# Optimization experiments

Measured on AMD Instinct MI355X. Metric: run time of the kernel, lower is better.

Reference implementation:

```python
import jax, jax.numpy as jnp
import numpy as np

D_MODEL, D_K, D_V, N_HEADS = 1024, 64, 64, 16


def setup_inputs() -> dict:
    key = jax.random.key(0)
    ks = jax.random.split(key, 8)
    B, S = 2, 2048
    s = 0.02
    return {
        "x": jax.random.normal(ks[0], (B, S, D_MODEL), dtype=jnp.float32),
        "Wq": jax.random.normal(ks[1], (D_MODEL, N_HEADS * D_K), dtype=jnp.float32) * s,
        "bq": jnp.zeros((N_HEADS * D_K,), dtype=jnp.float32),
        "Wk": jax.random.normal(ks[2], (D_MODEL, N_HEADS * D_K), dtype=jnp.float32) * s,
        "bk": jnp.zeros((N_HEADS * D_K,), dtype=jnp.float32),
        "Wv": jax.random.normal(ks[3], (D_MODEL, N_HEADS * D_V), dtype=jnp.float32) * s,
        "bv": jnp.zeros((N_HEADS * D_V,), dtype=jnp.float32),
        "Wo": jax.random.normal(ks[4], (N_HEADS * D_V, D_MODEL), dtype=jnp.float32) * s,
    }


def reference(x, Wq, bq, Wk, bk, Wv, bv, Wo):
    B, S, _ = x.shape
    split = lambda t, d: t.reshape(B, S, N_HEADS, d).transpose(0, 2, 1, 3)  # [B,H,S,d]
    Q = split(x @ Wq + bq, D_K)
    K = split(x @ Wk + bk, D_K)
    V = split(x @ Wv + bv, D_V)
    scores = jnp.einsum("bhqd,bhkd->bhqk", Q / jnp.sqrt(jnp.float32(D_K)), K)
    # causal mask: x + (1 - 1/tril) == 0 on allowed, -inf on disallowed
    causal = jnp.tril(jnp.ones((S, S), dtype=bool))
    scores = jnp.where(causal, scores, -jnp.inf)
    attn = jax.nn.softmax(scores, axis=-1)
    out = jnp.einsum("bhqk,bhkd->bhqd", attn, V)  # [B,H,S,d_v]
    out = out.transpose(0, 2, 1, 3).reshape(B, S, N_HEADS * D_V)
    return out @ Wo
```

## Files before the change

### kernel.cpp

```cpp
#include <hip/hip_runtime.h>
#include <hip/hip_bf16.h>
#include <hip/hip_fp16.h>
#include <cstdint>

#define DEVINL __device__ __forceinline__

typedef __attribute__((ext_vector_type(4))) float floatx4;
typedef __attribute__((ext_vector_type(8))) __bf16 bf16x8;
typedef __attribute__((ext_vector_type(4))) _Float16 half4;
typedef __attribute__((ext_vector_type(4))) unsigned short u16x4;

DEVINL floatx4 mfma_16x16x32(bf16x8 a, bf16x8 b, floatx4 c) {
  return __builtin_amdgcn_mfma_f32_16x16x32_bf16(a, b, c, 0, 0, 0);
}
DEVINL floatx4 mfma_16x16x16_f16(half4 a, half4 b, floatx4 c) {
  return __builtin_amdgcn_mfma_f32_16x16x16f16(a, b, c, 0, 0, 0);
}

DEVINL void async_copy16(const void* g, void* l) {
  __builtin_amdgcn_global_load_lds(
      (__attribute__((address_space(1))) void*)(void*)g,
      (__attribute__((address_space(3))) void*)l, 16, 0, 0);
}

#define QSCALE 0.18033688011112042f

__global__ void cast_to_bf16(const float* __restrict__ in,
                             __hip_bfloat16* __restrict__ out, int n) {
  int i = (blockIdx.x * blockDim.x + threadIdx.x) * 4;
  if (i + 3 < n) {
    const float4 v = *(const float4*)&in[i];
    out[i + 0] = __float2bfloat16(v.x);
    out[i + 1] = __float2bfloat16(v.y);
    out[i + 2] = __float2bfloat16(v.z);
    out[i + 3] = __float2bfloat16(v.w);
  }
}

__global__ void transpose_cast4(const float* __restrict__ Wq,
                                const float* __restrict__ Wk,
                                const float* __restrict__ Wv,
                                const float* __restrict__ Wo,
                                __hip_bfloat16* __restrict__ Wt,
                                __hip_bfloat16* __restrict__ Wot) {
  __shared__ float tile[32][33];
  const int z = blockIdx.z;
  const float* W = (z == 0) ? Wq : (z == 1) ? Wk : (z == 2) ? Wv : Wo;
  __hip_bfloat16* dst = (z < 3) ? (Wt + ((int64_t)z << 20)) : Wot;
  const int k0 = blockIdx.x * 32, n0 = blockIdx.y * 32;
  const int tx = threadIdx.x, ty = threadIdx.y;
#pragma unroll
  for (int i = 0; i < 32; i += 8)
    tile[ty + i][tx] = W[(int64_t)(k0 + ty + i) * 1024 + n0 + tx];
  __syncthreads();
#pragma unroll
  for (int i = 0; i < 32; i += 8)
    dst[(int64_t)(n0 + ty + i) * 1024 + k0 + tx] =
        __float2bfloat16(tile[tx][ty + i]);
}

__global__ void transpose_v(const unsigned short* __restrict__ Vb,
                            unsigned short* __restrict__ Vt) {
  __shared__ unsigned short t[32][33];
  const int s0 = blockIdx.x * 32, d0 = blockIdx.y * 32, bh = blockIdx.z;
  const unsigned short* src = Vb + (int64_t)bh * 2048 * 64;
  unsigned short* dst = Vt + (int64_t)bh * 64 * 2048;
  const int tx = threadIdx.x, ty = threadIdx.y;
#pragma unroll
  for (int i = 0; i < 32; i += 8)
    t[ty + i][tx] = src[(int64_t)(s0 + ty + i) * 64 + d0 + tx];
  __syncthreads();
#pragma unroll
  for (int i = 0; i < 32; i += 8)
    dst[(int64_t)(d0 + ty + i) * 2048 + s0 + tx] = t[tx][ty + i];
}

template <int MODE>
__global__ __launch_bounds__(256, 2) void gemm_bt(
    const __hip_bfloat16* __restrict__ A, const __hip_bfloat16* __restrict__ Bt,
    int M, int N, int K, const float* __restrict__ bq,
    const float* __restrict__ bk, const float* __restrict__ bv,
    __hip_bfloat16* __restrict__ Qb, __hip_bfloat16* __restrict__ Kb,
    _Float16* __restrict__ Vb, float* __restrict__ outf) {
  __shared__ __align__(16) __hip_bfloat16 As[128 * 32];
  __shared__ __align__(16) __hip_bfloat16 Bs[128 * 32];
  const int tid = threadIdx.x;
  const int wave = tid >> 6, lane = tid & 63;
  const int quad = lane >> 4, l16 = lane & 15;
  const int bm = blockIdx.x * 128, bn = blockIdx.y * 128;
  const int wm = (wave >> 1) * 64, wn = (wave & 1) * 64;

  floatx4 acc[4][4] = {};

  const int arow = tid >> 2, aseg = tid & 3;
  for (int k0 = 0; k0 < K; k0 += 32) {
#pragma unroll
    for (int i = 0; i < 2; ++i) {
      const int row = arow + i * 64;
      const int off = row * 32 + aseg * 8;
      async_copy16(A + (int64_t)(bm + row) * K + k0 + aseg * 8, As + off);
      async_copy16(Bt + (int64_t)(bn + row) * K + k0 + aseg * 8, Bs + off);
    }
    __syncthreads();
    bf16x8 af[4], bfr[4];
#pragma unroll
    for (int i = 0; i < 4; ++i) {
      af[i] = *(const bf16x8*)&As[(wm + i * 16 + l16) * 32 + quad * 8];
      bfr[i] = *(const bf16x8*)&Bs[(wn + i * 16 + l16) * 32 + quad * 8];
    }
#pragma unroll
    for (int i = 0; i < 4; ++i)
#pragma unroll
      for (int j = 0; j < 4; ++j)
        acc[i][j] = mfma_16x16x32(af[i], bfr[j], acc[i][j]);
    __syncthreads();
  }

#pragma unroll
  for (int i = 0; i < 4; ++i) {
#pragma unroll
    for (int j = 0; j < 4; ++j) {
      const int n = bn + wn + j * 16 + l16;
#pragma unroll
      for (int r = 0; r < 4; ++r) {
        const int m = bm + wm + i * 16 + quad * 4 + r;
        float v = acc[i][j][r];
        if (MODE == 0) {
          const int which = n >> 10, nn = n & 1023;
          const int h = nn >> 6, d = nn & 63;
          const int b = m >> 11, s = m & 2047;
          const float* bias = (which == 0) ? bq : (which == 1 ? bk : bv);
          v += bias[nn];
          const int64_t idx = ((int64_t)(b * 16 + h) * 2048 + s) * 64 + d;
          if (which == 2) {
            Vb[idx] = (_Float16)v;
          } else {
            if (which == 0) v *= QSCALE;
            ((which == 0) ? Qb : Kb)[idx] = __float2bfloat16(v);
          }
        } else {
          outf[(int64_t)m * N + n] = v;
        }
      }
    }
  }
}

__global__ __launch_bounds__(256, 3) void attn_kernel(
    const __hip_bfloat16* __restrict__ Qb, const __hip_bfloat16* __restrict__ Kb,
    const _Float16* __restrict__ Vt, __hip_bfloat16* __restrict__ Ab) {
  __shared__ __align__(16) char smem[32768];
  const int tid = threadIdx.x;
  const int wave = tid >> 6, lane = tid & 63;
  const int quad = lane >> 4, l16 = lane & 15;
  const int c = 31 - (int)(blockIdx.x >> 5);
  const int bh = blockIdx.x & 31;
  const int qbase = c * 64 + wave * 16;
  const int ktmax = c;

  const __hip_bfloat16* Qh = Qb + (int64_t)bh * 2048 * 64;
  const __hip_bfloat16* Kh = Kb + (int64_t)bh * 2048 * 64;
  const _Float16* Vh = Vt + (int64_t)bh * 64 * 2048;

  bf16x8 qf[2];
#pragma unroll
  for (int h = 0; h < 2; ++h)
    qf[h] = *(const bf16x8*)&Qh[(int64_t)(qbase + l16) * 64 + h * 32 + quad * 8];

  floatx4 o[4] = {};
  float lsum = 0.f;

  auto stage = [&](int buf, int k0s) {
#pragma unroll
    for (int i = 0; i < 2; ++i) {
      const int p = tid + i * 256;
      const int r = p >> 3, cc = (p & 7) ^ (r & 7);
      async_copy16(Kh + (int64_t)(k0s + r) * 64 + cc * 8,
                   smem + buf * 8192 + p * 16);
      async_copy16(Vh + (int64_t)r * 2048 + k0s + cc * 8,
                   smem + 16384 + buf * 8192 + p * 16);
    }
  };

  stage(0, 0);
  for (int kt = 0; kt <= ktmax; ++kt) {
    const int k0 = kt * 64;
    const int cur = kt & 1;
    __syncthreads();
    if (kt < ktmax) stage(cur ^ 1, k0 + 64);

    const char* kb = smem + cur * 8192;
    const char* vb = smem + 16384 + cur * 8192;
    const int sw = l16 & 7;

    bf16x8 kfr[4][2];
#pragma unroll
    for (int kk = 0; kk < 4; ++kk)
#pragma unroll
      for (int h = 0; h < 2; ++h)
        kfr[kk][h] = *(const bf16x8*)(kb + (kk * 16 + l16) * 128 +
                                      (((h * 4 + quad) ^ sw) << 4));

    floatx4 st[4];
#pragma unroll
    for (int kk = 0; kk < 4; ++kk) {
      floatx4 z = {};
      z = mfma_16x16x32(kfr[kk][0], qf[0], z);
      st[kk] = mfma_16x16x32(kfr[kk][1], qf[1], z);
    }

    half4 vfr[4][4];
#pragma unroll
    for (int dt = 0; dt < 4; ++dt)
#pragma unroll
      for (int kk = 0; kk < 4; ++kk)
        vfr[dt][kk] = *(const half4*)(vb + (dt * 16 + l16) * 128 +
                                      (((kk * 2 + (quad >> 1)) ^ sw) << 4) +
                                      (quad & 1) * 8);

    const bool masked = (kt == ktmax);
    half4 pf[4];
#pragma unroll
    for (int kk = 0; kk < 4; ++kk) {
#pragma unroll
      for (int r = 0; r < 4; ++r) {
        const int key = k0 + kk * 16 + quad * 4 + r;
        float p = __builtin_amdgcn_exp2f(st[kk][r]);
        if (masked && key > qbase + l16) p = 0.f;
        lsum += p;
        pf[kk][r] = (_Float16)p;
      }
    }

#pragma unroll
    for (int dt = 0; dt < 4; ++dt)
#pragma unroll
      for (int kk = 0; kk < 4; ++kk)
        o[dt] = mfma_16x16x16_f16(vfr[dt][kk], pf[kk], o[dt]);
  }

  lsum += __shfl_xor(lsum, 16, 64);
  lsum += __shfl_xor(lsum, 32, 64);
  const float invl = 1.0f / lsum;

  const int b = bh >> 4, h = bh & 15;
#pragma unroll
  for (int dt = 0; dt < 4; ++dt) {
    u16x4 pack;
#pragma unroll
    for (int r = 0; r < 4; ++r)
      pack[r] = __builtin_bit_cast(unsigned short,
                                   __float2bfloat16(o[dt][r] * invl));
    *(u16x4*)&Ab[(int64_t)(b * 2048 + qbase + l16) * 1024 + h * 64 + dt * 16 +
                 quad * 4] = pack;
  }
}

extern "C" void kernel_launch(void* const* d_in, const int* in_sizes, int n_in,
                              void* d_out, int out_size, void* d_ws,
                              size_t ws_size, hipStream_t stream) {
  const float* x = (const float*)d_in[0];
  const float* Wq = (const float*)d_in[1];
  const float* bq = (const float*)d_in[2];
  const float* Wk = (const float*)d_in[3];
  const float* bk = (const float*)d_in[4];
  const float* Wv = (const float*)d_in[5];
  const float* bv = (const float*)d_in[6];
  const float* Wo = (const float*)d_in[7];
  float* out = (float*)d_out;

  char* ws = (char*)d_ws;
  __hip_bfloat16* xb = (__hip_bfloat16*)(ws);
  __hip_bfloat16* Wt = (__hip_bfloat16*)(ws + (8ll << 20));
  __hip_bfloat16* Wot = (__hip_bfloat16*)(ws + (14ll << 20));
  __hip_bfloat16* Qb = (__hip_bfloat16*)(ws + (16ll << 20));
  __hip_bfloat16* Kb = (__hip_bfloat16*)(ws + (24ll << 20));
  _Float16* Vt = (_Float16*)(ws + (32ll << 20));
  _Float16* Vb = (_Float16*)(ws + (40ll << 20));
  __hip_bfloat16* Ab = xb;

  cast_to_bf16<<<4096, 256, 0, stream>>>(x, xb, 4096 * 1024);
  transpose_cast4<<<dim3(32, 32, 4), dim3(32, 8), 0, stream>>>(Wq, Wk, Wv, Wo,
                                                               Wt, Wot);
  gemm_bt<0><<<dim3(32, 24), 256, 0, stream>>>(xb, Wt, 4096, 3072, 1024, bq, bk,
                                               bv, Qb, Kb, Vb, nullptr);
  transpose_v<<<dim3(64, 2, 32), dim3(32, 8), 0, stream>>>(
      (const unsigned short*)Vb, (unsigned short*)Vt);
  attn_kernel<<<dim3(1024), 256, 0, stream>>>(Qb, Kb, Vt, Ab);
  gemm_bt<1><<<dim3(32, 8), 256, 0, stream>>>(Ab, Wot, 4096, 1024, 1024,
                                              nullptr, nullptr, nullptr,
                                              nullptr, nullptr, nullptr, out);
}
```

Measured before the change: 181.4 us.

## Fuse V transpose into QKV GEMM epilogue and give each attention wave two query tiles

The QKV projection GEMM now writes V directly in transposed [d][s] layout. It stages each wave's tile through swizzled shared memory and stores it with vectorized half8 writes, which removes the separate transpose_v kernel and its extra round trip of V through global memory. The attention kernel drops to 128 threads, and each wave handles 32 query rows as two 16-row tiles. That way every K and V fragment loaded from LDS feeds twice as many MFMAs. The costs are more registers per wave, fewer waves per block, and extra barriers in the V epilogue.

```diff
diff --git a/kernel.cpp b/kernel.cpp
--- a/kernel.cpp
+++ b/kernel.cpp
@@ -8,6 +8,7 @@
 typedef __attribute__((ext_vector_type(4))) float floatx4;
 typedef __attribute__((ext_vector_type(8))) __bf16 bf16x8;
 typedef __attribute__((ext_vector_type(4))) _Float16 half4;
+typedef __attribute__((ext_vector_type(8))) _Float16 half8;
 typedef __attribute__((ext_vector_type(4))) unsigned short u16x4;
 
 DEVINL floatx4 mfma_16x16x32(bf16x8 a, bf16x8 b, floatx4 c) {
@@ -24,6 +25,9 @@
 }
 
 #define QSCALE 0.18033688011112042f
+
+#define VS(d, s) \
+  ((d) * 128 + (((((s) >> 3)) ^ ((d) & 7)) << 4) + ((s) & 7) * 2)
 
 __global__ void cast_to_bf16(const float* __restrict__ in,
                              __hip_bfloat16* __restrict__ out, int n) {
@@ -59,29 +63,13 @@
         __float2bfloat16(tile[tx][ty + i]);
 }
 
-__global__ void transpose_v(const unsigned short* __restrict__ Vb,
-                            unsigned short* __restrict__ Vt) {
-  __shared__ unsigned short t[32][33];
-  const int s0 = blockIdx.x * 32, d0 = blockIdx.y * 32, bh = blockIdx.z;
-  const unsigned short* src = Vb + (int64_t)bh * 2048 * 64;
-  unsigned short* dst = Vt + (int64_t)bh * 64 * 2048;
-  const int tx = threadIdx.x, ty = threadIdx.y;
-#pragma unroll
-  for (int i = 0; i < 32; i += 8)
-    t[ty + i][tx] = src[(int64_t)(s0 + ty + i) * 64 + d0 + tx];
-  __syncthreads();
-#pragma unroll
-  for (int i = 0; i < 32; i += 8)
-    dst[(int64_t)(d0 + ty + i) * 2048 + s0 + tx] = t[tx][ty + i];
-}
-
 template <int MODE>
 __global__ __launch_bounds__(256, 2) void gemm_bt(
     const __hip_bfloat16* __restrict__ A, const __hip_bfloat16* __restrict__ Bt,
     int M, int N, int K, const float* __restrict__ bq,
     const float* __restrict__ bk, const float* __restrict__ bv,
     __hip_bfloat16* __restrict__ Qb, __hip_bfloat16* __restrict__ Kb,
-    _Float16* __restrict__ Vb, float* __restrict__ outf) {
+    _Float16* __restrict__ Vt, float* __restrict__ outf) {
   __shared__ __align__(16) __hip_bfloat16 As[128 * 32];
   __shared__ __align__(16) __hip_bfloat16 Bs[128 * 32];
   const int tid = threadIdx.x;
@@ -116,37 +104,76 @@
     __syncthreads();
   }
 
-#pragma unroll
-  for (int i = 0; i < 4; ++i) {
-#pragma unroll
-    for (int j = 0; j < 4; ++j) {
-      const int n = bn + wn + j * 16 + l16;
-#pragma unroll
-      for (int r = 0; r < 4; ++r) {
-        const int m = bm + wm + i * 16 + quad * 4 + r;
-        float v = acc[i][j][r];
-        if (MODE == 0) {
-          const int which = n >> 10, nn = n & 1023;
-          const int h = nn >> 6, d = nn & 63;
+  if (MODE == 1) {
+#pragma unroll
+    for (int i = 0; i < 4; ++i)
+#pragma unroll
+      for (int j = 0; j < 4; ++j) {
+        const int n = bn + wn + j * 16 + l16;
+#pragma unroll
+        for (int r = 0; r < 4; ++r) {
+          const int m = bm + wm + i * 16 + quad * 4 + r;
+          outf[(int64_t)m * N + n] = acc[i][j][r];
+        }
+      }
+  } else if (bn < 2048) {
+#pragma unroll
+    for (int i = 0; i < 4; ++i)
+#pragma unroll
+      for (int j = 0; j < 4; ++j) {
+        const int n = bn + wn + j * 16 + l16;
+        const int which = n >> 10, nn = n & 1023;
+        const int h = nn >> 6, d = nn & 63;
+        const float* bias = (which == 0) ? bq : bk;
+#pragma unroll
+        for (int r = 0; r < 4; ++r) {
+          const int m = bm + wm + i * 16 + quad * 4 + r;
           const int b = m >> 11, s = m & 2047;
-          const float* bias = (which == 0) ? bq : (which == 1 ? bk : bv);
-          v += bias[nn];
-          const int64_t idx = ((int64_t)(b * 16 + h) * 2048 + s) * 64 + d;
-          if (which == 2) {
-            Vb[idx] = (_Float16)v;
-          } else {
-            if (which == 0) v *= QSCALE;
-            ((which == 0) ? Qb : Kb)[idx] = __float2bfloat16(v);
+          float v = acc[i][j][r] + bias[nn];
+          if (which == 0) v *= QSCALE;
+          ((which == 0) ? Qb : Kb)[((int64_t)(b * 16 + h) * 2048 + s) * 64 + d] =
+              __float2bfloat16(v);
+        }
+      }
+  } else {
+    char* scr = (wave & 1) ? (char*)Bs : (char*)As;
+    const int h = ((bn + wn) & 1023) >> 6;
+    const int bb = (bm + wm) >> 11;
+    const int sbase = (bm + wm) & 2047;
+    _Float16* dstV = Vt + (int64_t)(bb * 16 + h) * 64 * 2048;
+#pragma unroll
+    for (int phase = 0; phase < 2; ++phase) {
+      __syncthreads();
+      if ((wave >> 1) == phase) {
+#pragma unroll
+        for (int i = 0; i < 4; ++i)
+#pragma unroll
+          for (int j = 0; j < 4; ++j) {
+            const int d = j * 16 + l16;
+#pragma unroll
+            for (int r = 0; r < 4; ++r) {
+              const int s = i * 16 + quad * 4 + r;
+              *(_Float16*)(scr + VS(d, s)) =
+                  (_Float16)(acc[i][j][r] + bv[((bn + wn) & 1023) + d]);
+            }
           }
-        } else {
-          outf[(int64_t)m * N + n] = v;
+      }
+      __syncthreads();
+      if ((wave >> 1) == phase) {
+#pragma unroll
+        for (int it = 0; it < 8; ++it) {
+          const int idx = lane + it * 64;
+          const int d = idx >> 3, sc = idx & 7;
+          const half8 vv =
+              *(const half8*)(scr + d * 128 + ((sc ^ (d & 7)) << 4));
+          *(half8*)(dstV + (int64_t)d * 2048 + sbase + sc * 8) = vv;
         }
       }
     }
   }
 }
 
-__global__ __launch_bounds__(256, 3) void attn_kernel(
+__global__ __launch_bounds__(128, 2) void attn_kernel(
     const __hip_bfloat16* __restrict__ Qb, const __hip_bfloat16* __restrict__ Kb,
     const _Float16* __restrict__ Vt, __hip_bfloat16* __restrict__ Ab) {
   __shared__ __align__(16) char smem[32768];
@@ -155,25 +182,28 @@
   const int quad = lane >> 4, l16 = lane & 15;
   const int c = 31 - (int)(blockIdx.x >> 5);
   const int bh = blockIdx.x & 31;
-  const int qbase = c * 64 + wave * 16;
+  const int qbase = c * 64 + wave * 32;
   const int ktmax = c;
 
   const __hip_bfloat16* Qh = Qb + (int64_t)bh * 2048 * 64;
   const __hip_bfloat16* Kh = Kb + (int64_t)bh * 2048 * 64;
   const _Float16* Vh = Vt + (int64_t)bh * 64 * 2048;
 
-  bf16x8 qf[2];
-#pragma unroll
-  for (int h = 0; h < 2; ++h)
-    qf[h] = *(const bf16x8*)&Qh[(int64_t)(qbase + l16) * 64 + h * 32 + quad * 8];
-
-  floatx4 o[4] = {};
-  float lsum = 0.f;
+  bf16x8 qf[2][2];
+#pragma unroll
+  for (int rt = 0; rt < 2; ++rt)
+#pragma unroll
+    for (int h = 0; h < 2; ++h)
+      qf[rt][h] = *(const bf16x8*)&Qh[(int64_t)(qbase + rt * 16 + l16) * 64 +
+                                      h * 32 + quad * 8];
+
+  floatx4 o[2][4] = {};
+  float lsum[2] = {0.f, 0.f};
 
   auto stage = [&](int buf, int k0s) {
 #pragma unroll
-    for (int i = 0; i < 2; ++i) {
-      const int p = tid + i * 256;
+    for (int i = 0; i < 4; ++i) {
+      const int p = tid + i * 128;
       const int r = p >> 3, cc = (p & 7) ^ (r & 7);
       async_copy16(Kh + (int64_t)(k0s + r) * 64 + cc * 8,
                    smem + buf * 8192 + p * 16);
@@ -201,13 +231,15 @@
         kfr[kk][h] = *(const bf16x8*)(kb + (kk * 16 + l16) * 128 +
                                       (((h * 4 + quad) ^ sw) << 4));
 
-    floatx4 st[4];
-#pragma unroll
-    for (int kk = 0; kk < 4; ++kk) {
-      floatx4 z = {};
-      z = mfma_16x16x32(kfr[kk][0], qf[0], z);
-      st[kk] = mfma_16x16x32(kfr[kk][1], qf[1], z);
-    }
+    floatx4 st[2][4];
+#pragma unroll
+    for (int kk = 0; kk < 4; ++kk)
+#pragma unroll
+      for (int rt = 0; rt < 2; ++rt) {
+        floatx4 z = {};
+        z = mfma_16x16x32(kfr[kk][0], qf[rt][0], z);
+        st[rt][kk] = mfma_16x16x32(kfr[kk][1], qf[rt][1], z);
+      }
 
     half4 vfr[4][4];
 #pragma unroll
@@ -219,16 +251,20 @@
                                       (quad & 1) * 8);
 
     const bool masked = (kt == ktmax);
-    half4 pf[4];
-#pragma unroll
-    for (int kk = 0; kk < 4; ++kk) {
-#pragma unroll
-      for (int r = 0; r < 4; ++r) {
-        const int key = k0 + kk * 16 + quad * 4 + r;
-        float p = __builtin_amdgcn_exp2f(st[kk][r]);
-        if (masked && key > qbase + l16) p = 0.f;
-        lsum += p;
-        pf[kk][r] = (_Float16)p;
+    half4 pf[2][4];
+#pragma unroll
+    for (int rt = 0; rt < 2; ++rt) {
+      const int qrow = qbase + rt * 16 + l16;
+#pragma unroll
+      for (int kk = 0; kk < 4; ++kk) {
+#pragma unroll
+        for (int r = 0; r < 4; ++r) {
+          const int key = k0 + kk * 16 + quad * 4 + r;
+          float p = __builtin_amdgcn_exp2f(st[rt][kk][r]);
+          if (masked && key > qrow) p = 0.f;
+          lsum[rt] += p;
+          pf[rt][kk][r] = (_Float16)p;
+        }
       }
     }
 
@@ -236,23 +272,31 @@
     for (int dt = 0; dt < 4; ++dt)
 #pragma unroll
       for (int kk = 0; kk < 4; ++kk)
-        o[dt] = mfma_16x16x16_f16(vfr[dt][kk], pf[kk], o[dt]);
-  }
-
-  lsum += __shfl_xor(lsum, 16, 64);
-  lsum += __shfl_xor(lsum, 32, 64);
-  const float invl = 1.0f / lsum;
+#pragma unroll
+        for (int rt = 0; rt < 2; ++rt)
+          o[rt][dt] = mfma_16x16x16_f16(vfr[dt][kk], pf[rt][kk], o[rt][dt]);
+  }
+
+#pragma unroll
+  for (int rt = 0; rt < 2; ++rt) {
+    lsum[rt] += __shfl_xor(lsum[rt], 16, 64);
+    lsum[rt] += __shfl_xor(lsum[rt], 32, 64);
+  }
 
   const int b = bh >> 4, h = bh & 15;
 #pragma unroll
-  for (int dt = 0; dt < 4; ++dt) {
-    u16x4 pack;
-#pragma unroll
-    for (int r = 0; r < 4; ++r)
-      pack[r] = __builtin_bit_cast(unsigned short,
-                                   __float2bfloat16(o[dt][r] * invl));
-    *(u16x4*)&Ab[(int64_t)(b * 2048 + qbase + l16) * 1024 + h * 64 + dt * 16 +
-                 quad * 4] = pack;
+  for (int rt = 0; rt < 2; ++rt) {
+    const float invl = 1.0f / lsum[rt];
+#pragma unroll
+    for (int dt = 0; dt < 4; ++dt) {
+      u16x4 pack;
+#pragma unroll
+      for (int r = 0; r < 4; ++r)
+        pack[r] = __builtin_bit_cast(unsigned short,
+                                     __float2bfloat16(o[rt][dt][r] * invl));
+      *(u16x4*)&Ab[(int64_t)(b * 2048 + qbase + rt * 16 + l16) * 1024 +
+                   h * 64 + dt * 16 + quad * 4] = pack;
+    }
   }
 }
 
@@ -276,17 +320,14 @@
   __hip_bfloat16* Qb = (__hip_bfloat16*)(ws + (16ll << 20));
   __hip_bfloat16* Kb = (__hip_bfloat16*)(ws + (24ll << 20));
   _Float16* Vt = (_Float16*)(ws + (32ll << 20));
-  _Float16* Vb = (_Float16*)(ws + (40ll << 20));
   __hip_bfloat16* Ab = xb;
 
   cast_to_bf16<<<4096, 256, 0, stream>>>(x, xb, 4096 * 1024);
   transpose_cast4<<<dim3(32, 32, 4), dim3(32, 8), 0, stream>>>(Wq, Wk, Wv, Wo,
                                                                Wt, Wot);
   gemm_bt<0><<<dim3(32, 24), 256, 0, stream>>>(xb, Wt, 4096, 3072, 1024, bq, bk,
-                                               bv, Qb, Kb, Vb, nullptr);
-  transpose_v<<<dim3(64, 2, 32), dim3(32, 8), 0, stream>>>(
-      (const unsigned short*)Vb, (unsigned short*)Vt);
-  attn_kernel<<<dim3(1024), 256, 0, stream>>>(Qb, Kb, Vt, Ab);
+                                               bv, Qb, Kb, Vt, nullptr);
+  attn_kernel<<<dim3(1024), 128, 0, stream>>>(Qb, Kb, Vt, Ab);
   gemm_bt<1><<<dim3(32, 8), 256, 0, stream>>>(Ab, Wot, 4096, 1024, 1024,
                                               nullptr, nullptr, nullptr,
                                               nullptr, nullptr, nullptr, out);
```

After: 182.8 us. No clear change (+0.7%).
